# Kernel optimization log

Hardware: AMD Instinct MI355X
Metric: run time of the kernel (lower is better)

The kernel has to match this reference:

```python
import jax, jax.numpy as jnp
import numpy as np

B, D_IN, D_HID, D_OUT, E, TOP_K = 4096, 1024, 4096, 1024, 8, 2


def setup_inputs() -> dict:
    key = jax.random.key(0)
    ks = jax.random.split(key, 7)
    s_in = 1.0 / np.sqrt(D_IN)
    s_hid = 1.0 / np.sqrt(D_HID)
    return {
        "x": jax.random.normal(ks[0], (B, D_IN), jnp.float32),
        "Wg": jax.random.uniform(ks[1], (D_IN, E), jnp.float32, -s_in, s_in),
        "bg": jax.random.uniform(ks[2], (E,), jnp.float32, -s_in, s_in),
        "W1": jax.random.uniform(ks[3], (E, D_IN, D_HID), jnp.float32, -s_in, s_in),
        "b1": jax.random.uniform(ks[4], (E, D_HID), jnp.float32, -s_in, s_in),
        "W2": jax.random.uniform(ks[5], (E, D_HID, D_OUT), jnp.float32, -s_hid, s_hid),
        "b2": jax.random.uniform(ks[6], (E, D_OUT), jnp.float32, -s_hid, s_hid),
    }


def reference(x, Wg, bg, W1, b1, W2, b2):
    # Gating: [B, E]
    gate_logits = x @ Wg + bg
    # Top-k routing (values sorted descending, same as torch.topk)
    topk_logits, topk_idx = jax.lax.top_k(gate_logits, TOP_K)  # [B, K]
    topk_w = jax.nn.softmax(topk_logits, axis=-1)  # [B, K]

    # Dense per-expert FFN for all tokens (reference form of grouped GEMM)
    h = jax.nn.relu(jnp.einsum("bi,eih->beh", x, W1) + b1[None])  # [B, E, H]
    y = jnp.einsum("beh,eho->beo", h, W2) + b2[None]              # [B, E, O]

    # Gather selected experts' outputs and combine with routing weights
    y_sel = jnp.take_along_axis(y, topk_idx[:, :, None], axis=1)  # [B, K, O]
    output = jnp.sum(topk_w[:, :, None] * y_sel, axis=1)          # [B, O]

    # Load-balance auxiliary loss
    gates = jax.nn.softmax(gate_logits, axis=-1)
    expert_usage = gates.mean(axis=0)
    load_balance_loss = E * jnp.sum(expert_usage ** 2)
    return output, load_balance_loss
```

## Files before the change

### kernel.cpp

```cpp
#include <hip/hip_runtime.h>
#include <hip/hip_fp16.h>

#define BTOK  4096
#define D_IN  1024
#define D_HID 4096
#define D_OUT 1024
#define NE    8
#define PT_MAX 72
#define P_MAX  9216
#define HHALF  2048
#define KT1    32
#define NT1    16
#define KT2    64
#define NT2    8

typedef _Float16 half8 __attribute__((ext_vector_type(8)));
typedef _Float16 half4v __attribute__((ext_vector_type(4)));
typedef float    floatx4 __attribute__((ext_vector_type(4)));


__device__ __forceinline__ void g2l16(const void* g, void* s) {
    __builtin_amdgcn_global_load_lds((const __attribute__((address_space(1))) void*)g,
                                     (__attribute__((address_space(3))) void*)s, 16, 0, 0);
}

__global__ void gating_kernel(const float* __restrict__ x, const float* __restrict__ Wg,
                              const float* __restrict__ bg,
                              int* __restrict__ t2i, float* __restrict__ t2w,
                              int* __restrict__ cnt, float* __restrict__ usage) {
    __shared__ float susage[NE];
    int tid = threadIdx.x;
    if (tid < NE) susage[tid] = 0.f;
    __syncthreads();
    int wv = tid >> 6, lane = tid & 63;
    int t = blockIdx.x * 4 + wv;
    double part[NE];
    #pragma unroll
    for (int e = 0; e < NE; ++e) part[e] = 0.0;
    for (int i = lane; i < D_IN; i += 64) {
        double xv = (double)x[(size_t)t * D_IN + i];
        #pragma unroll
        for (int e = 0; e < NE; ++e) part[e] += xv * (double)Wg[i * NE + e];
    }
    #pragma unroll
    for (int e = 0; e < NE; ++e) {
        #pragma unroll
        for (int s = 32; s > 0; s >>= 1) part[e] += __shfl_xor(part[e], s, 64);
    }
    if (lane == 0) {
        float l[NE];
        #pragma unroll
        for (int e = 0; e < NE; ++e) l[e] = (float)part[e] + bg[e];
        float M = l[0];
        #pragma unroll
        for (int e = 1; e < NE; ++e) M = fmaxf(M, l[e]);
        float s = 0.f, g[NE];
        #pragma unroll
        for (int e = 0; e < NE; ++e) { g[e] = __expf(l[e] - M); s += g[e]; }
        float inv = 1.f / s;
        #pragma unroll
        for (int e = 0; e < NE; ++e) atomicAdd(&susage[e], g[e] * inv);
        int i0 = 0; float b0 = l[0];
        #pragma unroll
        for (int e = 1; e < NE; ++e) if (l[e] > b0) { b0 = l[e]; i0 = e; }
        int i1 = -1; float b1v = -1e30f;
        #pragma unroll
        for (int e = 0; e < NE; ++e) if (e != i0 && l[e] > b1v) { b1v = l[e]; i1 = e; }
        float w0 = 1.f / (1.f + expf(b1v - b0));
        t2i[2 * t] = i0; t2i[2 * t + 1] = i1;
        t2w[2 * t] = w0; t2w[2 * t + 1] = 1.f - w0;
        atomicAdd(&cnt[i0], 1);
        atomicAdd(&cnt[i1], 1);
    }
    __syncthreads();
    if (tid < NE) atomicAdd(&usage[tid], susage[tid]);
}

__global__ void scan_kernel(int* __restrict__ meta, float* __restrict__ out_loss) {
    if (threadIdx.x != 0) return;
    int* cnt = meta; int* cursor = meta + 8; int* offs = meta + 16;
    int* tile2e = meta + 24; int* ntiles = meta + 96;
    float* usage = (float*)(meta + 100);
    int run = 0;
    for (int e = 0; e < NE; ++e) {
        offs[e] = run; cursor[e] = run;
        int ntl = (cnt[e] + 127) >> 7;
        int t0 = run >> 7;
        for (int i = 0; i < ntl; ++i) tile2e[t0 + i] = e;
        run += ntl << 7;
    }
    ntiles[0] = run >> 7;
    float loss = 0.f;
    for (int e = 0; e < NE; ++e) { float u = usage[e] / (float)BTOK; loss += u * u; }
    out_loss[0] = (float)NE * loss;
}

__global__ void fill_kernel(int* __restrict__ ptok) {
    ptok[blockIdx.x * 256 + threadIdx.x] = 0;
}

__global__ void scatter_kernel(const int* __restrict__ t2i, int* __restrict__ cursor,
                               int* __restrict__ ptok, int* __restrict__ pslot) {
    int t = blockIdx.x * blockDim.x + threadIdx.x;
    if (t >= BTOK) return;
    #pragma unroll
    for (int k = 0; k < 2; ++k) {
        int e = t2i[2 * t + k];
        int slot = atomicAdd(&cursor[e], 1);
        ptok[slot] = t;
        pslot[2 * t + k] = slot;
    }
}

__global__ void gather_x_kernel(const float* __restrict__ x, const int* __restrict__ ptok,
                                _Float16* __restrict__ xt) {
    int k0 = blockIdx.x, ptile = blockIdx.y;
    int t = threadIdx.x;
    int m = t >> 1, kb = (t & 1) * 16;
    int tok = ptok[ptile * 128 + m];
    const float* src = x + (size_t)tok * D_IN + k0 * 32 + kb;
    float4 v0 = *(const float4*)(src);
    float4 v1 = *(const float4*)(src + 4);
    float4 v2 = *(const float4*)(src + 8);
    float4 v3 = *(const float4*)(src + 12);
    half8 o0, o1;
    o0[0]=(_Float16)v0.x; o0[1]=(_Float16)v0.y; o0[2]=(_Float16)v0.z; o0[3]=(_Float16)v0.w;
    o0[4]=(_Float16)v1.x; o0[5]=(_Float16)v1.y; o0[6]=(_Float16)v1.z; o0[7]=(_Float16)v1.w;
    o1[0]=(_Float16)v2.x; o1[1]=(_Float16)v2.y; o1[2]=(_Float16)v2.z; o1[3]=(_Float16)v2.w;
    o1[4]=(_Float16)v3.x; o1[5]=(_Float16)v3.y; o1[6]=(_Float16)v3.z; o1[7]=(_Float16)v3.w;
    _Float16* dst = xt + ((size_t)ptile * KT1 + k0) * 4096 + t * 16;
    *(half8*)dst = o0;
    *(half8*)(dst + 8) = o1;
}

__global__ void wtile_kernel(const float* __restrict__ W, _Float16* __restrict__ Wt,
                             int Ktot, int Ntot, int k_off, int n_off, int KT, int NT) {
    int k0 = blockIdx.x, ntb = blockIdx.y, e = blockIdx.z;
    int t = threadIdx.x;
    int nl = t >> 1, kb = (t & 1) * 16;
    const float* src = W + ((size_t)e * Ktot + k_off + k0 * 32 + kb) * Ntot
                         + n_off + ntb * 128 + nl;
    float v[16];
    #pragma unroll
    for (int j = 0; j < 16; ++j) v[j] = src[(size_t)j * Ntot];
    half8 o0, o1;
    #pragma unroll
    for (int j = 0; j < 8; ++j) { o0[j] = (_Float16)v[j]; o1[j] = (_Float16)v[j + 8]; }
    _Float16* dst = Wt + (((size_t)e * NT + ntb) * KT + k0) * 4096 + t * 16;
    *(half8*)dst = o0;
    *(half8*)(dst + 8) = o1;
}

__global__ __launch_bounds__(256)
void gemm1_kernel(const _Float16* __restrict__ xt, const _Float16* __restrict__ W1t,
                  const float* __restrict__ b1, _Float16* __restrict__ ht,
                  const int* __restrict__ meta, int n_off) {
    int ptile = blockIdx.x;
    if (ptile >= meta[96]) return;
    int nt = blockIdx.y;
    int e = meta[24 + ptile];

    __shared__ __align__(16) _Float16 Asm[128 * 32];
    __shared__ __align__(16) _Float16 Bsm[128 * 32];

    int tid = threadIdx.x;
    int wave = tid >> 6, lane = tid & 63;
    const _Float16* Abase = xt + (size_t)ptile * KT1 * 4096;
    const _Float16* Bbase = W1t + ((size_t)(e * NT1 + nt) * KT1) * 4096;
    int stg = wave * 512 + lane * 8;

    floatx4 acc[4][4] = {};
    int lr = lane & 15, lq = lane >> 4;
    int wm = (wave & 1) * 64, wn = (wave >> 1) * 64;

    for (int k0 = 0; k0 < KT1; ++k0) {
        __syncthreads();
        const _Float16* aG = Abase + (size_t)k0 * 4096 + stg;
        const _Float16* bG = Bbase + (size_t)k0 * 4096 + stg;
        g2l16(aG,        &Asm[wave * 512]);
        g2l16(aG + 2048, &Asm[wave * 512 + 2048]);
        g2l16(bG,        &Bsm[wave * 512]);
        g2l16(bG + 2048, &Bsm[wave * 512 + 2048]);
        __syncthreads();
        half8 af[4], bf[4];
        #pragma unroll
        for (int f = 0; f < 4; ++f) {
            af[f] = *(const half8*)&Asm[(wm + f * 16 + lr) * 32 + lq * 8];
            bf[f] = *(const half8*)&Bsm[(wn + f * 16 + lr) * 32 + lq * 8];
        }
        #pragma unroll
        for (int mf = 0; mf < 4; ++mf)
            #pragma unroll
            for (int nf = 0; nf < 4; ++nf)
                acc[mf][nf] = __builtin_amdgcn_mfma_f32_16x16x32_f16(af[mf], bf[nf], acc[mf][nf], 0, 0, 0);
    }

    const float* b1e = b1 + (size_t)e * D_HID + n_off;
    #pragma unroll
    for (int mf = 0; mf < 4; ++mf) {
        #pragma unroll
        for (int v = 0; v < 4; ++v) {
            int m = wm + mf * 16 + lq * 4 + v;
            #pragma unroll
            for (int nf = 0; nf < 4; ++nf) {
                int hl = nt * 128 + wn + nf * 16 + lr;
                float val = acc[mf][nf][v] + b1e[hl];
                ht[((size_t)ptile * KT2 + (hl >> 5)) * 4096 + m * 32 + (hl & 31)]
                    = (_Float16)fmaxf(val, 0.f);
            }
        }
    }
}

__global__ __launch_bounds__(256)
void gemm2_kernel(const _Float16* __restrict__ ht, const _Float16* __restrict__ W2t,
                  _Float16* __restrict__ y, const int* __restrict__ meta) {
    int ptile = blockIdx.x;
    if (ptile >= meta[96]) return;
    int nt = blockIdx.y;
    int e = meta[24 + ptile];

    __shared__ __align__(16) _Float16 Asm[128 * 32];
    __shared__ __align__(16) _Float16 Bsm[128 * 32];

    int tid = threadIdx.x;
    int wave = tid >> 6, lane = tid & 63;
    const _Float16* Abase = ht + (size_t)ptile * KT2 * 4096;
    const _Float16* Bbase = W2t + ((size_t)(e * NT2 + nt) * KT2) * 4096;
    int stg = wave * 512 + lane * 8;

    floatx4 acc[4][4] = {};
    int lr = lane & 15, lq = lane >> 4;
    int wm = (wave & 1) * 64, wn = (wave >> 1) * 64;

    for (int k0 = 0; k0 < KT2; ++k0) {
        __syncthreads();
        const _Float16* aG = Abase + (size_t)k0 * 4096 + stg;
        const _Float16* bG = Bbase + (size_t)k0 * 4096 + stg;
        g2l16(aG,        &Asm[wave * 512]);
        g2l16(aG + 2048, &Asm[wave * 512 + 2048]);
        g2l16(bG,        &Bsm[wave * 512]);
        g2l16(bG + 2048, &Bsm[wave * 512 + 2048]);
        __syncthreads();
        half8 af[4], bf[4];
        #pragma unroll
        for (int f = 0; f < 4; ++f) {
            af[f] = *(const half8*)&Asm[(wm + f * 16 + lr) * 32 + lq * 8];
            bf[f] = *(const half8*)&Bsm[(wn + f * 16 + lr) * 32 + lq * 8];
        }
        #pragma unroll
        for (int mf = 0; mf < 4; ++mf)
            #pragma unroll
            for (int nf = 0; nf < 4; ++nf)
                acc[mf][nf] = __builtin_amdgcn_mfma_f32_16x16x32_f16(af[mf], bf[nf], acc[mf][nf], 0, 0, 0);
    }

    #pragma unroll
    for (int mf = 0; mf < 4; ++mf) {
        #pragma unroll
        for (int v = 0; v < 4; ++v) {
            int m = wm + mf * 16 + lq * 4 + v;
            #pragma unroll
            for (int nf = 0; nf < 4; ++nf) {
                int c = nt * 128 + wn + nf * 16 + lr;
                y[(size_t)(ptile * 128 + m) * D_OUT + c] = (_Float16)acc[mf][nf][v];
            }
        }
    }
}

__global__ void combine_kernel(const _Float16* __restrict__ yA, const _Float16* __restrict__ yB,
                               const float* __restrict__ b2, const int* __restrict__ t2i,
                               const float* __restrict__ t2w, const int* __restrict__ pslot,
                               float* __restrict__ out) {
    int t = blockIdx.x;
    int c = threadIdx.x * 4;
    int e0 = t2i[2 * t], e1 = t2i[2 * t + 1];
    float w0 = t2w[2 * t], w1 = t2w[2 * t + 1];
    size_t s0 = (size_t)pslot[2 * t] * D_OUT + c;
    size_t s1 = (size_t)pslot[2 * t + 1] * D_OUT + c;
    half4v a0 = *(const half4v*)(yA + s0);
    half4v b0 = *(const half4v*)(yB + s0);
    half4v a1 = *(const half4v*)(yA + s1);
    half4v b1v = *(const half4v*)(yB + s1);
    float4 bias0 = *(const float4*)(b2 + (size_t)e0 * D_OUT + c);
    float4 bias1 = *(const float4*)(b2 + (size_t)e1 * D_OUT + c);
    float4 o;
    o.x = w0 * ((float)a0[0] + (float)b0[0] + bias0.x) + w1 * ((float)a1[0] + (float)b1v[0] + bias1.x);
    o.y = w0 * ((float)a0[1] + (float)b0[1] + bias0.y) + w1 * ((float)a1[1] + (float)b1v[1] + bias1.y);
    o.z = w0 * ((float)a0[2] + (float)b0[2] + bias0.z) + w1 * ((float)a1[2] + (float)b1v[2] + bias1.z);
    o.w = w0 * ((float)a0[3] + (float)b0[3] + bias0.w) + w1 * ((float)a1[3] + (float)b1v[3] + bias1.w);
    *(float4*)(out + (size_t)t * D_OUT + c) = o;
}

extern "C" void kernel_launch(void* const* d_in, const int* in_sizes, int n_in,
                              void* d_out, int out_size, void* d_ws, size_t ws_size,
                              hipStream_t stream) {
    const float* x  = (const float*)d_in[0];
    const float* Wg = (const float*)d_in[1];
    const float* bg = (const float*)d_in[2];
    const float* W1 = (const float*)d_in[3];
    const float* b1 = (const float*)d_in[4];
    const float* W2 = (const float*)d_in[5];
    const float* b2 = (const float*)d_in[6];
    float* out = (float*)d_out;

    char* ws = (char*)d_ws;
    _Float16* xt    = (_Float16*)(ws);
    _Float16* Wt    = (_Float16*)(ws + 18874368ull);
    _Float16* ht    = (_Float16*)(ws + 52428800ull);
    _Float16* yA    = (_Float16*)(ws + 90177536ull);
    _Float16* yB    = (_Float16*)(ws + 109051904ull);
    int*      t2i   = (int*)(ws + 127926272ull);
    float*    t2w   = (float*)(ws + 127959040ull);
    int*      ptok  = (int*)(ws + 127991808ull);
    int*      pslot = (int*)(ws + 128028672ull);
    int*      meta  = (int*)(ws + 128061440ull);
    int* cnt = meta; int* cursor = meta + 8;
    float* usage = (float*)(meta + 100);

    hipMemsetAsync(meta, 0, 512, stream);

    gating_kernel<<<1024, 256, 0, stream>>>(x, Wg, bg, t2i, t2w, cnt, usage);
    scan_kernel<<<1, 64, 0, stream>>>(meta, out + (size_t)BTOK * D_OUT);
    fill_kernel<<<36, 256, 0, stream>>>(ptok);
    scatter_kernel<<<16, 256, 0, stream>>>(t2i, cursor, ptok, pslot);
    gather_x_kernel<<<dim3(KT1, PT_MAX), 256, 0, stream>>>(x, ptok, xt);

    wtile_kernel<<<dim3(KT1, NT1, 8), 256, 0, stream>>>(W1, Wt, D_IN, D_HID, 0, 0, KT1, NT1);
    gemm1_kernel<<<dim3(PT_MAX, NT1), 256, 0, stream>>>(xt, Wt, b1, ht, meta, 0);
    wtile_kernel<<<dim3(KT2, NT2, 8), 256, 0, stream>>>(W2, Wt, D_HID, D_OUT, 0, 0, KT2, NT2);
    gemm2_kernel<<<dim3(PT_MAX, NT2), 256, 0, stream>>>(ht, Wt, yA, meta);

    wtile_kernel<<<dim3(KT1, NT1, 8), 256, 0, stream>>>(W1, Wt, D_IN, D_HID, 0, HHALF, KT1, NT1);
    gemm1_kernel<<<dim3(PT_MAX, NT1), 256, 0, stream>>>(xt, Wt, b1, ht, meta, HHALF);
    wtile_kernel<<<dim3(KT2, NT2, 8), 256, 0, stream>>>(W2, Wt, D_HID, D_OUT, HHALF, 0, KT2, NT2);
    gemm2_kernel<<<dim3(PT_MAX, NT2), 256, 0, stream>>>(ht, Wt, yB, meta);

    combine_kernel<<<BTOK, 256, 0, stream>>>(yA, yB, b2, t2i, t2w, pslot, out);
}
```

Baseline: 691.7 us.

## Stage gating weights in LDS, replace global atomics with per-block partials

```diff
diff --git a/kernel.cpp b/kernel.cpp
--- a/kernel.cpp
+++ b/kernel.cpp
@@ -13,6 +13,7 @@
 #define NT1    16
 #define KT2    64
 #define NT2    8
+#define GB     256
 
 typedef _Float16 half8 __attribute__((ext_vector_type(8)));
 typedef _Float16 half4v __attribute__((ext_vector_type(4)));
@@ -24,75 +25,101 @@
                                      (__attribute__((address_space(3))) void*)s, 16, 0, 0);
 }
 
-__global__ void gating_kernel(const float* __restrict__ x, const float* __restrict__ Wg,
-                              const float* __restrict__ bg,
-                              int* __restrict__ t2i, float* __restrict__ t2w,
-                              int* __restrict__ cnt, float* __restrict__ usage) {
+__global__ __launch_bounds__(256)
+void gating_kernel(const float* __restrict__ x, const float* __restrict__ Wg,
+                   const float* __restrict__ bg,
+                   int* __restrict__ t2i, float* __restrict__ t2w,
+                   int* __restrict__ pcnt, float* __restrict__ pusage) {
+    __shared__ float wgT[NE * 1024];
     __shared__ float susage[NE];
+    __shared__ int   scnt[NE];
     int tid = threadIdx.x;
-    if (tid < NE) susage[tid] = 0.f;
+    if (tid < NE) { susage[tid] = 0.f; scnt[tid] = 0; }
+    #pragma unroll
+    for (int k = 0; k < 8192; k += 256) {
+        int idx = k + tid;
+        wgT[(idx & 7) * 1024 + (idx >> 3)] = Wg[idx];
+    }
     __syncthreads();
     int wv = tid >> 6, lane = tid & 63;
-    int t = blockIdx.x * 4 + wv;
-    double part[NE];
-    #pragma unroll
-    for (int e = 0; e < NE; ++e) part[e] = 0.0;
-    for (int i = lane; i < D_IN; i += 64) {
-        double xv = (double)x[(size_t)t * D_IN + i];
-        #pragma unroll
-        for (int e = 0; e < NE; ++e) part[e] += xv * (double)Wg[i * NE + e];
-    }
-    #pragma unroll
-    for (int e = 0; e < NE; ++e) {
-        #pragma unroll
-        for (int s = 32; s > 0; s >>= 1) part[e] += __shfl_xor(part[e], s, 64);
-    }
+    for (int tt = 0; tt < 4; ++tt) {
+        int t = blockIdx.x * 16 + wv * 4 + tt;
+        double part[NE];
+        #pragma unroll
+        for (int e = 0; e < NE; ++e) part[e] = 0.0;
+        #pragma unroll
+        for (int j = 0; j < 16; ++j) {
+            int i = j * 64 + lane;
+            double xv = (double)x[(size_t)t * D_IN + i];
+            #pragma unroll
+            for (int e = 0; e < NE; ++e) part[e] += xv * (double)wgT[e * 1024 + i];
+        }
+        #pragma unroll
+        for (int e = 0; e < NE; ++e) {
+            #pragma unroll
+            for (int s = 32; s > 0; s >>= 1) part[e] += __shfl_xor(part[e], s, 64);
+        }
+        if (lane == 0) {
+            float l[NE];
+            #pragma unroll
+            for (int e = 0; e < NE; ++e) l[e] = (float)part[e] + bg[e];
+            float M = l[0];
+            #pragma unroll
+            for (int e = 1; e < NE; ++e) M = fmaxf(M, l[e]);
+            float s = 0.f, g[NE];
+            #pragma unroll
+            for (int e = 0; e < NE; ++e) { g[e] = __expf(l[e] - M); s += g[e]; }
+            float inv = 1.f / s;
+            #pragma unroll
+            for (int e = 0; e < NE; ++e) atomicAdd(&susage[e], g[e] * inv);
+            int i0 = 0; float b0 = l[0];
+            #pragma unroll
+            for (int e = 1; e < NE; ++e) if (l[e] > b0) { b0 = l[e]; i0 = e; }
+            int i1 = -1; float b1v = -1e30f;
+            #pragma unroll
+            for (int e = 0; e < NE; ++e) if (e != i0 && l[e] > b1v) { b1v = l[e]; i1 = e; }
+            float w0 = 1.f / (1.f + expf(b1v - b0));
+            t2i[2 * t] = i0; t2i[2 * t + 1] = i1;
+            t2w[2 * t] = w0; t2w[2 * t + 1] = 1.f - w0;
+            atomicAdd(&scnt[i0], 1);
+            atomicAdd(&scnt[i1], 1);
+        }
+    }
+    __syncthreads();
+    if (tid < NE) {
+        pcnt[blockIdx.x * NE + tid] = scnt[tid];
+        pusage[blockIdx.x * NE + tid] = susage[tid];
+    }
+}
+
+__global__ void scan_kernel(const int* __restrict__ pcnt, const float* __restrict__ pusage,
+                            int* __restrict__ meta, float* __restrict__ out_loss) {
+    int lane = threadIdx.x;
+    int e = lane & 7, b0 = lane >> 3;
+    int c = 0; float u = 0.f;
+    for (int b = b0; b < GB; b += 8) { c += pcnt[b * 8 + e]; u += pusage[b * 8 + e]; }
+    #pragma unroll
+    for (int s = 8; s < 64; s <<= 1) { c += __shfl_xor(c, s, 64); u += __shfl_xor(u, s, 64); }
+    int cAll[NE]; float uAll[NE];
+    #pragma unroll
+    for (int q = 0; q < NE; ++q) { cAll[q] = __shfl(c, q, 64); uAll[q] = __shfl(u, q, 64); }
     if (lane == 0) {
-        float l[NE];
-        #pragma unroll
-        for (int e = 0; e < NE; ++e) l[e] = (float)part[e] + bg[e];
-        float M = l[0];
-        #pragma unroll
-        for (int e = 1; e < NE; ++e) M = fmaxf(M, l[e]);
-        float s = 0.f, g[NE];
-        #pragma unroll
-        for (int e = 0; e < NE; ++e) { g[e] = __expf(l[e] - M); s += g[e]; }
-        float inv = 1.f / s;
-        #pragma unroll
-        for (int e = 0; e < NE; ++e) atomicAdd(&susage[e], g[e] * inv);
-        int i0 = 0; float b0 = l[0];
-        #pragma unroll
-        for (int e = 1; e < NE; ++e) if (l[e] > b0) { b0 = l[e]; i0 = e; }
-        int i1 = -1; float b1v = -1e30f;
-        #pragma unroll
-        for (int e = 0; e < NE; ++e) if (e != i0 && l[e] > b1v) { b1v = l[e]; i1 = e; }
-        float w0 = 1.f / (1.f + expf(b1v - b0));
-        t2i[2 * t] = i0; t2i[2 * t + 1] = i1;
-        t2w[2 * t] = w0; t2w[2 * t + 1] = 1.f - w0;
-        atomicAdd(&cnt[i0], 1);
-        atomicAdd(&cnt[i1], 1);
-    }
-    __syncthreads();
-    if (tid < NE) atomicAdd(&usage[tid], susage[tid]);
-}
-
-__global__ void scan_kernel(int* __restrict__ meta, float* __restrict__ out_loss) {
-    if (threadIdx.x != 0) return;
-    int* cnt = meta; int* cursor = meta + 8; int* offs = meta + 16;
-    int* tile2e = meta + 24; int* ntiles = meta + 96;
-    float* usage = (float*)(meta + 100);
-    int run = 0;
-    for (int e = 0; e < NE; ++e) {
-        offs[e] = run; cursor[e] = run;
-        int ntl = (cnt[e] + 127) >> 7;
-        int t0 = run >> 7;
-        for (int i = 0; i < ntl; ++i) tile2e[t0 + i] = e;
-        run += ntl << 7;
-    }
-    ntiles[0] = run >> 7;
-    float loss = 0.f;
-    for (int e = 0; e < NE; ++e) { float u = usage[e] / (float)BTOK; loss += u * u; }
-    out_loss[0] = (float)NE * loss;
+        int* cnt = meta; int* cursor = meta + 8; int* offs = meta + 16;
+        int* tile2e = meta + 24; int* ntiles = meta + 96;
+        int run = 0;
+        for (int q = 0; q < NE; ++q) {
+            cnt[q] = cAll[q];
+            offs[q] = run; cursor[q] = run;
+            int ntl = (cAll[q] + 127) >> 7;
+            int tb = run >> 7;
+            for (int i = 0; i < ntl; ++i) tile2e[tb + i] = q;
+            run += ntl << 7;
+        }
+        ntiles[0] = run >> 7;
+        float loss = 0.f;
+        for (int q = 0; q < NE; ++q) { float uu = uAll[q] / (float)BTOK; loss += uu * uu; }
+        out_loss[0] = (float)NE * loss;
+    }
 }
 
 __global__ void fill_kernel(int* __restrict__ ptok) {
@@ -101,15 +128,20 @@
 
 __global__ void scatter_kernel(const int* __restrict__ t2i, int* __restrict__ cursor,
                                int* __restrict__ ptok, int* __restrict__ pslot) {
-    int t = blockIdx.x * blockDim.x + threadIdx.x;
-    if (t >= BTOK) return;
-    #pragma unroll
-    for (int k = 0; k < 2; ++k) {
-        int e = t2i[2 * t + k];
-        int slot = atomicAdd(&cursor[e], 1);
-        ptok[slot] = t;
-        pslot[2 * t + k] = slot;
-    }
+    __shared__ int lcnt[NE], base[NE];
+    int tid = threadIdx.x;
+    if (tid < NE) lcnt[tid] = 0;
+    __syncthreads();
+    int t = blockIdx.x * 256 + tid;
+    int e0 = t2i[2 * t], e1 = t2i[2 * t + 1];
+    int l0 = atomicAdd(&lcnt[e0], 1);
+    int l1 = atomicAdd(&lcnt[e1], 1);
+    __syncthreads();
+    if (tid < NE) base[tid] = atomicAdd(&cursor[tid], lcnt[tid]);
+    __syncthreads();
+    int s0 = base[e0] + l0, s1 = base[e1] + l1;
+    ptok[s0] = t; ptok[s1] = t;
+    pslot[2 * t] = s0; pslot[2 * t + 1] = s1;
 }
 
 __global__ void gather_x_kernel(const float* __restrict__ x, const int* __restrict__ ptok,
@@ -306,23 +338,24 @@
     float* out = (float*)d_out;
 
     char* ws = (char*)d_ws;
-    _Float16* xt    = (_Float16*)(ws);
-    _Float16* Wt    = (_Float16*)(ws + 18874368ull);
-    _Float16* ht    = (_Float16*)(ws + 52428800ull);
-    _Float16* yA    = (_Float16*)(ws + 90177536ull);
-    _Float16* yB    = (_Float16*)(ws + 109051904ull);
-    int*      t2i   = (int*)(ws + 127926272ull);
-    float*    t2w   = (float*)(ws + 127959040ull);
-    int*      ptok  = (int*)(ws + 127991808ull);
-    int*      pslot = (int*)(ws + 128028672ull);
-    int*      meta  = (int*)(ws + 128061440ull);
-    int* cnt = meta; int* cursor = meta + 8;
-    float* usage = (float*)(meta + 100);
+    _Float16* xt     = (_Float16*)(ws);
+    _Float16* Wt     = (_Float16*)(ws + 18874368ull);
+    _Float16* ht     = (_Float16*)(ws + 52428800ull);
+    _Float16* yA     = (_Float16*)(ws + 90177536ull);
+    _Float16* yB     = (_Float16*)(ws + 109051904ull);
+    int*      t2i    = (int*)(ws + 127926272ull);
+    float*    t2w    = (float*)(ws + 127959040ull);
+    int*      ptok   = (int*)(ws + 127991808ull);
+    int*      pslot  = (int*)(ws + 128028672ull);
+    int*      meta   = (int*)(ws + 128061440ull);
+    int*      pcnt   = (int*)(ws + 128061952ull);
+    float*    pusage = (float*)(ws + 128070144ull);
+    int* cursor = meta + 8;
 
     hipMemsetAsync(meta, 0, 512, stream);
 
-    gating_kernel<<<1024, 256, 0, stream>>>(x, Wg, bg, t2i, t2w, cnt, usage);
-    scan_kernel<<<1, 64, 0, stream>>>(meta, out + (size_t)BTOK * D_OUT);
+    gating_kernel<<<GB, 256, 0, stream>>>(x, Wg, bg, t2i, t2w, pcnt, pusage);
+    scan_kernel<<<1, 64, 0, stream>>>(pcnt, pusage, meta, out + (size_t)BTOK * D_OUT);
     fill_kernel<<<36, 256, 0, stream>>>(ptok);
     scatter_kernel<<<16, 256, 0, stream>>>(t2i, cursor, ptok, pslot);
     gather_x_kernel<<<dim3(KT1, PT_MAX), 256, 0, stream>>>(x, ptok, xt);
```

Result: faster. 575.4 us (-16.8%).
